# Optimization experiments

Hardware: AMD Instinct MI355X
Metric: run time of the kernel (lower is better)

Reference implementation:

```python
import jax, jax.numpy as jnp
import numpy as np

NE = 64        # num experts
H = 1024       # hidden_size
F = 2048       # ffn_hidden_size per expert
T = 16384      # total tokens


def setup_inputs() -> dict:
    key = jax.random.key(0)
    k1, k2, k3 = jax.random.split(key, 3)
    x = jax.random.normal(k1, (T, H), jnp.float32)
    w1 = jax.random.normal(k2, (NE, F, H), jnp.float32) * 0.02
    w2 = jax.random.normal(k3, (NE, F, H), jnp.float32) * 0.02
    # ragged token counts per expert, summing exactly to T
    rng = np.random.default_rng(0)
    sizes = rng.multinomial(T, np.ones(NE) / NE)
    tokens_per_expert = jnp.asarray(sizes, jnp.int32)
    return {"x": x, "w1": w1, "w2": w2, "tokens_per_expert": tokens_per_expert}


def _grouped_gmm(x, w, sizes, trans_b=False):
    # grouped GEMM: per-expert segment of x multiplied by that expert's weight.
    # sizes are concrete host ints (group boundaries are static), so we emit
    # one GEMM per expert with static slices, matching gg.ops.gmm semantics.
    offs = np.concatenate([[0], np.cumsum(sizes)]).astype(np.int64)
    outs = []
    for e in range(len(sizes)):
        xe = x[int(offs[e]):int(offs[e + 1])]          # [n_e, k]
        we = w[e].T if trans_b else w[e]               # [k, n]
        outs.append(xe @ we)
    return jnp.concatenate(outs, axis=0)


def reference(x, w1, w2, tokens_per_expert):
    sizes = np.asarray(tokens_per_expert)
    h = _grouped_gmm(x, w1, sizes, trans_b=True)       # [T, F]
    h = jax.nn.gelu(h, approximate=False)              # torch F.gelu (exact erf)
    return _grouped_gmm(h, w2, sizes, trans_b=False)   # [T, H]
```

## Files before the change

kernel.cpp:

```cpp
#include <hip/hip_runtime.h>
#include <hip/hip_bf16.h>

#define NE 64
#define HDIM 1024
#define FDIM 2048
#define TDIM 16384

typedef __attribute__((ext_vector_type(8))) short short8;
typedef __attribute__((ext_vector_type(4))) float f32x4;
typedef unsigned short u16;
typedef unsigned int u32;

__device__ __forceinline__ u16 bf16_rne(float f) {
  union { float f; u32 u; } a; a.f = f;
  u32 r = a.u + 0x7fffu + ((a.u >> 16) & 1u);
  return (u16)(r >> 16);
}

__global__ void k_prep(const int* __restrict__ tpe, int4* __restrict__ map,
                       int* __restrict__ nblocks) {
  if (threadIdx.x != 0 || blockIdx.x != 0) return;
  int off = 0, nb = 0;
  for (int e = 0; e < NE; ++e) {
    int n = tpe[e];
    for (int r = 0; r < n; r += 128) {
      int re = (r + 128 < n) ? (r + 128) : n;
      map[nb++] = make_int4(e, off + r, off + re, 0);
    }
    off += n;
  }
  *nblocks = nb;
}

__global__ void k_conv(const float4* __restrict__ in, uint2* __restrict__ out, int n4) {
  int stride = gridDim.x * blockDim.x;
  for (int i = blockIdx.x * blockDim.x + threadIdx.x; i < n4; i += stride) {
    float4 v = in[i];
    uint2 o;
    o.x = bf16_rne(v.x) | ((u32)bf16_rne(v.y) << 16);
    o.y = bf16_rne(v.z) | ((u32)bf16_rne(v.w) << 16);
    out[i] = o;
  }
}

template<int K, int N, bool GELU, int BMODE>
__global__ __launch_bounds__(256) void k_gemm(
    const u16* __restrict__ A, const float* __restrict__ Bf, void* __restrict__ C,
    const int4* __restrict__ map, const int* __restrict__ nblocks)
{
  if ((int)blockIdx.x >= *nblocks) return;
  const int4 mi = map[blockIdx.x];
  const int e = mi.x, row0 = mi.y, rowend = mi.z;
  const int n0 = blockIdx.y << 7;

  __shared__ u16 smem[4096 + 128 * 40];

  const int tid = threadIdx.x;
  const int wid = tid >> 6, lane = tid & 63;
  const int wr = wid >> 1, wc = wid & 1;
  const int fr = lane & 15, fq = lane >> 4;

  f32x4 acc[4][4];
#pragma unroll
  for (int m = 0; m < 4; ++m)
#pragma unroll
    for (int n = 0; n < 4; ++n) acc[m][n] = (f32x4)0.f;

  const float* B = Bf + (size_t)e * ((size_t)N * K);

  for (int k0 = 0; k0 < K; k0 += 32) {
#pragma unroll
    for (int i = 0; i < 2; ++i) {
      int slot = i * 256 + tid;
      int row = row0 + (slot >> 2);
      row = row < TDIM ? row : TDIM - 1;
      const u16* g = A + (size_t)row * K + k0 + (slot & 3) * 8;
      __builtin_amdgcn_global_load_lds(
          (const __attribute__((address_space(1))) u32*)g,
          (__attribute__((address_space(3))) u32*)(smem + i * 2048 + wid * 512),
          16, 0, 0);
    }
    if constexpr (BMODE == 1) {
      float4 v[4];
#pragma unroll
      for (int i = 0; i < 4; ++i) {
        int slot = i * 256 + tid;
        v[i] = *(const float4*)(B + (size_t)(n0 + (slot >> 3)) * K + k0 + (slot & 7) * 4);
      }
#pragma unroll
      for (int i = 0; i < 4; ++i) {
        int slot = i * 256 + tid;
        uint2 o;
        o.x = bf16_rne(v[i].x) | ((u32)bf16_rne(v[i].y) << 16);
        o.y = bf16_rne(v[i].z) | ((u32)bf16_rne(v[i].w) << 16);
        *(uint2*)(smem + 4096 + (slot >> 3) * 40 + (slot & 7) * 4) = o;
      }
    } else {
      const int nn = ((wid & 1) << 6) | lane;
      const int g  = wid >> 1;
      const float* src = B + (size_t)(k0 + g * 16) * N + n0 + nn;
      float v[16];
#pragma unroll
      for (int i = 0; i < 16; ++i) v[i] = src[(size_t)i * N];
      short8 lo, hi;
#pragma unroll
      for (int i = 0; i < 8; ++i) {
        lo[i] = (short)bf16_rne(v[i]);
        hi[i] = (short)bf16_rne(v[i + 8]);
      }
      *(short8*)(smem + 4096 + nn * 40 + g * 16 + 0) = lo;
      *(short8*)(smem + 4096 + nn * 40 + g * 16 + 8) = hi;
    }
    __syncthreads();

    short8 av[4], bv[4];
#pragma unroll
    for (int m = 0; m < 4; ++m)
      av[m] = *(const short8*)(smem + (wr * 64 + m * 16 + fr) * 32 + fq * 8);
#pragma unroll
    for (int n = 0; n < 4; ++n)
      bv[n] = *(const short8*)(smem + 4096 + (wc * 64 + n * 16 + fr) * 40 + fq * 8);
#pragma unroll
    for (int m = 0; m < 4; ++m)
#pragma unroll
      for (int n = 0; n < 4; ++n)
        acc[m][n] = __builtin_amdgcn_mfma_f32_16x16x32_bf16(av[m], bv[n], acc[m][n], 0, 0, 0);
    __syncthreads();
  }

#pragma unroll
  for (int m = 0; m < 4; ++m) {
    const int rb = row0 + wr * 64 + m * 16 + fq * 4;
#pragma unroll
    for (int n = 0; n < 4; ++n) {
      const int col = n0 + wc * 64 + n * 16 + fr;
#pragma unroll
      for (int j = 0; j < 4; ++j) {
        int r = rb + j;
        if (r < rowend) {
          float vv = acc[m][n][j];
          if constexpr (GELU) {
            vv = 0.5f * vv * (1.f + erff(vv * 0.70710678118654752f));
            ((u16*)C)[(size_t)r * N + col] = bf16_rne(vv);
          } else {
            ((float*)C)[(size_t)r * N + col] = vv;
          }
        }
      }
    }
  }
}

extern "C" void kernel_launch(void* const* d_in, const int* in_sizes, int n_in,
                              void* d_out, int out_size, void* d_ws, size_t ws_size,
                              hipStream_t stream) {
  const float* x  = (const float*)d_in[0];
  const float* w1 = (const float*)d_in[1];
  const float* w2 = (const float*)d_in[2];
  const int*  tpe = (const int*)d_in[3];

  char* ws = (char*)d_ws;
  int4* map     = (int4*)ws;
  int*  nblocks = (int*)(ws + 4096);
  u16*  xb      = (u16*)(ws + 8192);
  u16*  hb      = xb + (size_t)TDIM * HDIM;

  k_prep<<<1, 64, 0, stream>>>(tpe, map, nblocks);
  k_conv<<<2048, 256, 0, stream>>>((const float4*)x, (uint2*)xb, (TDIM * HDIM) / 4);
  k_gemm<HDIM, FDIM, true,  1><<<dim3(192, FDIM / 128), 256, 0, stream>>>(
      xb, w1, (void*)hb, map, nblocks);
  k_gemm<FDIM, HDIM, false, 2><<<dim3(192, HDIM / 128), 256, 0, stream>>>(
      hb, w2, d_out, map, nblocks);
}
```

Baseline: 541.5 us.

## Double-buffer LDS tiles and prefetch next K-slice during MFMA in grouped GEMM

Splits shared memory into two A and two B buffers. The next K-tile's A async loads and B global loads are issued before the current tile's MFMAs, and the converted B is written to the other buffer afterwards, which halves the barriers per iteration and hides global latency. The second GEMM's B load changes from 16 scalar strided loads to 8 float2 loads with packed uint4 LDS stores. The hand-written bf16 rounding is replaced with the __float2bfloat16 intrinsic. The cost is double the LDS use and more live registers, which may reduce occupancy.

```diff
diff --git a/kernel.cpp b/kernel.cpp
--- a/kernel.cpp
+++ b/kernel.cpp
@@ -11,10 +11,11 @@
 typedef unsigned short u16;
 typedef unsigned int u32;
 
-__device__ __forceinline__ u16 bf16_rne(float f) {
-  union { float f; u32 u; } a; a.f = f;
-  u32 r = a.u + 0x7fffu + ((a.u >> 16) & 1u);
-  return (u16)(r >> 16);
+__device__ __forceinline__ u16 f2bf(float f) {
+  return __bfloat16_as_ushort(__float2bfloat16(f));
+}
+__device__ __forceinline__ u32 pk2(float a, float b) {
+  return (u32)f2bf(a) | ((u32)f2bf(b) << 16);
 }
 
 __global__ void k_prep(const int* __restrict__ tpe, int4* __restrict__ map,
@@ -37,8 +38,8 @@
   for (int i = blockIdx.x * blockDim.x + threadIdx.x; i < n4; i += stride) {
     float4 v = in[i];
     uint2 o;
-    o.x = bf16_rne(v.x) | ((u32)bf16_rne(v.y) << 16);
-    o.y = bf16_rne(v.z) | ((u32)bf16_rne(v.w) << 16);
+    o.x = pk2(v.x, v.y);
+    o.y = pk2(v.z, v.w);
     out[i] = o;
   }
 }
@@ -52,8 +53,10 @@
   const int4 mi = map[blockIdx.x];
   const int e = mi.x, row0 = mi.y, rowend = mi.z;
   const int n0 = blockIdx.y << 7;
+  const int NT = K / 32;
 
-  __shared__ u16 smem[4096 + 128 * 40];
+  __shared__ u16 sa[2][4096];
+  __shared__ u16 sb[2][128 * 40];
 
   const int tid = threadIdx.x;
   const int wid = tid >> 6, lane = tid & 63;
@@ -68,63 +71,82 @@
 
   const float* B = Bf + (size_t)e * ((size_t)N * K);
 
-  for (int k0 = 0; k0 < K; k0 += 32) {
+  float4 v1[4];
+  float2 v2[8];
+  const int np2 = (tid & 63) << 1;
+  const int oct = tid >> 6;
+
+  auto issueA = [&](int t, int buf) {
 #pragma unroll
     for (int i = 0; i < 2; ++i) {
       int slot = i * 256 + tid;
       int row = row0 + (slot >> 2);
       row = row < TDIM ? row : TDIM - 1;
-      const u16* g = A + (size_t)row * K + k0 + (slot & 3) * 8;
+      const u16* g = A + (size_t)row * K + t * 32 + (slot & 3) * 8;
       __builtin_amdgcn_global_load_lds(
           (const __attribute__((address_space(1))) u32*)g,
-          (__attribute__((address_space(3))) u32*)(smem + i * 2048 + wid * 512),
+          (__attribute__((address_space(3))) u32*)(&sa[buf][i * 2048 + wid * 512]),
           16, 0, 0);
     }
+  };
+  auto loadB = [&](int t) {
     if constexpr (BMODE == 1) {
-      float4 v[4];
 #pragma unroll
       for (int i = 0; i < 4; ++i) {
         int slot = i * 256 + tid;
-        v[i] = *(const float4*)(B + (size_t)(n0 + (slot >> 3)) * K + k0 + (slot & 7) * 4);
+        v1[i] = *(const float4*)(B + (size_t)(n0 + (slot >> 3)) * K + t * 32 + (slot & 7) * 4);
       }
+    } else {
+      const float* src = B + (size_t)(t * 32 + oct * 8) * N + n0 + np2;
+#pragma unroll
+      for (int i = 0; i < 8; ++i) v2[i] = *(const float2*)(src + (size_t)i * N);
+    }
+  };
+  auto writeB = [&](int buf) {
+    if constexpr (BMODE == 1) {
 #pragma unroll
       for (int i = 0; i < 4; ++i) {
         int slot = i * 256 + tid;
         uint2 o;
-        o.x = bf16_rne(v[i].x) | ((u32)bf16_rne(v[i].y) << 16);
-        o.y = bf16_rne(v[i].z) | ((u32)bf16_rne(v[i].w) << 16);
-        *(uint2*)(smem + 4096 + (slot >> 3) * 40 + (slot & 7) * 4) = o;
+        o.x = pk2(v1[i].x, v1[i].y);
+        o.y = pk2(v1[i].z, v1[i].w);
+        *(uint2*)(&sb[buf][(slot >> 3) * 40 + (slot & 7) * 4]) = o;
       }
     } else {
-      const int nn = ((wid & 1) << 6) | lane;
-      const int g  = wid >> 1;
-      const float* src = B + (size_t)(k0 + g * 16) * N + n0 + nn;
-      float v[16];
-#pragma unroll
-      for (int i = 0; i < 16; ++i) v[i] = src[(size_t)i * N];
-      short8 lo, hi;
-#pragma unroll
-      for (int i = 0; i < 8; ++i) {
-        lo[i] = (short)bf16_rne(v[i]);
-        hi[i] = (short)bf16_rne(v[i + 8]);
-      }
-      *(short8*)(smem + 4096 + nn * 40 + g * 16 + 0) = lo;
-      *(short8*)(smem + 4096 + nn * 40 + g * 16 + 8) = hi;
+      uint4 c0, c1;
+      c0.x = pk2(v2[0].x, v2[1].x); c0.y = pk2(v2[2].x, v2[3].x);
+      c0.z = pk2(v2[4].x, v2[5].x); c0.w = pk2(v2[6].x, v2[7].x);
+      c1.x = pk2(v2[0].y, v2[1].y); c1.y = pk2(v2[2].y, v2[3].y);
+      c1.z = pk2(v2[4].y, v2[5].y); c1.w = pk2(v2[6].y, v2[7].y);
+      *(uint4*)(&sb[buf][np2 * 40 + oct * 8]) = c0;
+      *(uint4*)(&sb[buf][(np2 + 1) * 40 + oct * 8]) = c1;
     }
-    __syncthreads();
+  };
 
+  issueA(0, 0);
+  loadB(0);
+  writeB(0);
+  __syncthreads();
+
+  for (int t = 0; t < NT; ++t) {
+    const int cur = t & 1, nxt = cur ^ 1;
+    if (t + 1 < NT) {
+      issueA(t + 1, nxt);
+      loadB(t + 1);
+    }
     short8 av[4], bv[4];
 #pragma unroll
     for (int m = 0; m < 4; ++m)
-      av[m] = *(const short8*)(smem + (wr * 64 + m * 16 + fr) * 32 + fq * 8);
+      av[m] = *(const short8*)(&sa[cur][(wr * 64 + m * 16 + fr) * 32 + fq * 8]);
 #pragma unroll
     for (int n = 0; n < 4; ++n)
-      bv[n] = *(const short8*)(smem + 4096 + (wc * 64 + n * 16 + fr) * 40 + fq * 8);
+      bv[n] = *(const short8*)(&sb[cur][(wc * 64 + n * 16 + fr) * 40 + fq * 8]);
 #pragma unroll
     for (int m = 0; m < 4; ++m)
 #pragma unroll
       for (int n = 0; n < 4; ++n)
         acc[m][n] = __builtin_amdgcn_mfma_f32_16x16x32_bf16(av[m], bv[n], acc[m][n], 0, 0, 0);
+    if (t + 1 < NT) writeB(nxt);
     __syncthreads();
   }
 
@@ -141,7 +163,7 @@
           float vv = acc[m][n][j];
           if constexpr (GELU) {
             vv = 0.5f * vv * (1.f + erff(vv * 0.70710678118654752f));
-            ((u16*)C)[(size_t)r * N + col] = bf16_rne(vv);
+            ((u16*)C)[(size_t)r * N + col] = f2bf(vv);
           } else {
             ((float*)C)[(size_t)r * N + col] = vv;
           }
```

After: 560.3 us. 1.03x slower.
